# Optimization experiments

Measured on AMD Instinct MI355X. Metric: run time of the kernel, lower is better.

The kernel has to match this reference:

```python
import math
import jax, jax.numpy as jnp
import numpy as np

B, T, D, N_SLOTS, TOP_K = 4, 4096, 2048, 4096, 4


def setup_inputs() -> dict:
    key = jax.random.key(0)
    k1, k2, k3, k4, k5 = jax.random.split(key, 5)
    return {
        "x": jax.random.normal(k1, (B, T, D), dtype=jnp.float32),
        "slot_keys": jax.random.normal(k2, (N_SLOTS, D), dtype=jnp.float32) * 0.02,
        "slot_values": jax.random.normal(k3, (N_SLOTS, D), dtype=jnp.float32) * 0.02,
        "Wq": jax.random.normal(k4, (D, D), dtype=jnp.float32) * 0.02,
        "Wout": jax.random.normal(k5, (D, D), dtype=jnp.float32) * 0.02,
        "top_k": TOP_K,
    }


def reference(x, slot_keys, slot_values, Wq, Wout, top_k):
    d = x.shape[-1]
    scale = 1.0 / math.sqrt(d)
    q = jnp.einsum("btd,ed->bte", x, Wq)                 # proj_q (Linear, no bias)
    scores = jnp.einsum("btd,nd->btn", q, slot_keys) * scale  # [B,T,n_slots]
    topk_vals, topk_ids = jax.lax.top_k(scores, top_k)   # [B,T,k]
    attn = jax.nn.softmax(topk_vals, axis=-1)            # [B,T,k]
    gathered = slot_values[topk_ids]                     # [B,T,k,D] gather
    retrieved = jnp.einsum("btk,btkd->btd", attn, gathered)
    return jnp.einsum("btd,ed->bte", retrieved, Wout)    # proj_out
```

## Files before the change

kernel.cpp:

```cpp
#include <hip/hip_runtime.h>
#include <math.h>

#define D_DIM    2048
#define BT_DIM   16384
#define NSLOTS   4096
#define NTILES   32
#define SCALE    0.02209708691207961f
#define MARGIN   0.02f
#define CAND_MAX 16

typedef __attribute__((ext_vector_type(8))) short bf16x8;
typedef __attribute__((ext_vector_type(4))) float f32x4;
typedef __attribute__((ext_vector_type(8))) unsigned short u16x8;
typedef __attribute__((ext_vector_type(4))) unsigned short u16x4;

__device__ __forceinline__ unsigned short f2bf(float f) {
    unsigned int u = __float_as_uint(f);
    return (unsigned short)((u + 0x7fffu + ((u >> 16) & 1u)) >> 16);
}
__device__ __forceinline__ float bf2f(unsigned short s) {
    return __uint_as_float(((unsigned int)s) << 16);
}

__device__ __forceinline__ void async_cp16(const void* g, void* l) {
    __builtin_amdgcn_global_load_lds(
        (const __attribute__((address_space(1))) void*)g,
        (__attribute__((address_space(3))) void*)l, 16, 0, 0);
}

__device__ __forceinline__ bool cand_better(float v, int i, float v2, int i2) {
    return (v > v2) || (v == v2 && i < i2);
}

__device__ __forceinline__ void cand_insert(float v, int idx,
                                            float& v0, int& i0, float& v1, int& i1,
                                            float& v2, int& i2, float& v3, int& i3) {
    if (cand_better(v, idx, v3, i3)) {
        if (cand_better(v, idx, v0, i0)) {
            v3 = v2; i3 = i2; v2 = v1; i2 = i1; v1 = v0; i1 = i0; v0 = v; i0 = idx;
        } else if (cand_better(v, idx, v1, i1)) {
            v3 = v2; i3 = i2; v2 = v1; i2 = i1; v1 = v; i1 = idx;
        } else if (cand_better(v, idx, v2, i2)) {
            v3 = v2; i3 = i2; v2 = v; i2 = idx;
        } else {
            v3 = v; i3 = idx;
        }
    }
}

__device__ __forceinline__ void split3v(float v, unsigned short& h,
                                        unsigned short& m, unsigned short& l) {
    h = f2bf(v);
    const float r1 = v - bf2f(h);
    m = f2bf(r1);
    l = f2bf(r1 - bf2f(m));
}

__global__ __launch_bounds__(256)
void split3_lin(const float* __restrict__ in, unsigned short* __restrict__ oh,
                unsigned short* __restrict__ om, unsigned short* __restrict__ ol) {
    const size_t i = ((size_t)blockIdx.x * 256 + threadIdx.x) * 4;
    const float4 v = *(const float4*)(in + i);
    u16x4 h, m, l;
    unsigned short th, tm, tl;
    split3v(v.x, th, tm, tl); h[0] = th; m[0] = tm; l[0] = tl;
    split3v(v.y, th, tm, tl); h[1] = th; m[1] = tm; l[1] = tl;
    split3v(v.z, th, tm, tl); h[2] = th; m[2] = tm; l[2] = tl;
    split3v(v.w, th, tm, tl); h[3] = th; m[3] = tm; l[3] = tl;
    *(u16x4*)(oh + i) = h;
    *(u16x4*)(om + i) = m;
    *(u16x4*)(ol + i) = l;
}

__global__ __launch_bounds__(256)
void split3_wqT(const float* __restrict__ W, unsigned short* __restrict__ th,
                unsigned short* __restrict__ tm, unsigned short* __restrict__ tl) {
    __shared__ float tile[32][33];
    const int tx  = threadIdx.x & 31;
    const int ty4 = (threadIdx.x >> 5) * 4;
    const int e0  = blockIdx.y * 32;
    const int d0  = blockIdx.x * 32;
#pragma unroll
    for (int r = 0; r < 4; ++r)
        tile[ty4 + r][tx] = W[(size_t)(e0 + ty4 + r) * D_DIM + (d0 + tx)];
    __syncthreads();
#pragma unroll
    for (int r = 0; r < 4; ++r) {
        const float v = tile[tx][ty4 + r];
        unsigned short h, m, l;
        split3v(v, h, m, l);
        const size_t o = (size_t)(d0 + ty4 + r) * D_DIM + (e0 + tx);
        th[o] = h; tm[o] = m; tl[o] = l;
    }
}

__global__ __launch_bounds__(256)
void cvt_f32_bf16(const float* __restrict__ in, unsigned short* __restrict__ out) {
    const size_t i = ((size_t)blockIdx.x * 256 + threadIdx.x) * 8;
    float4 a = *(const float4*)(in + i);
    float4 b = *(const float4*)(in + i + 4);
    u16x8 o;
    o[0] = f2bf(a.x); o[1] = f2bf(a.y); o[2] = f2bf(a.z); o[3] = f2bf(a.w);
    o[4] = f2bf(b.x); o[5] = f2bf(b.y); o[6] = f2bf(b.z); o[7] = f2bf(b.w);
    *(u16x8*)(out + i) = o;
}

__global__ __launch_bounds__(256)
void gemm_kw_mfma6(const unsigned short* __restrict__ Ah,
                   const unsigned short* __restrict__ Am,
                   const unsigned short* __restrict__ Al,
                   const unsigned short* __restrict__ Bh,
                   const unsigned short* __restrict__ Bm,
                   const unsigned short* __restrict__ Bl,
                   float* __restrict__ KW, unsigned short* __restrict__ kwb,
                   int M, int N, int K) {
    __shared__ __align__(16) unsigned short AldsH[128 * 32];
    __shared__ __align__(16) unsigned short AldsM[128 * 32];
    __shared__ __align__(16) unsigned short AldsL[128 * 32];
    __shared__ __align__(16) unsigned short BldsH[128 * 32];
    __shared__ __align__(16) unsigned short BldsM[128 * 32];
    __shared__ __align__(16) unsigned short BldsL[128 * 32];

    const int tid  = threadIdx.x;
    const int lane = tid & 63;
    const int w    = tid >> 6;
    const int wr   = w >> 1, wc = w & 1;
    const int bmr  = blockIdx.y * 128;
    const int bnc  = blockIdx.x * 128;

    const int srow = lane >> 2;
    const int skch = (lane & 3) ^ ((lane >> 3) & 3);
    const int c0 = w, c1 = w + 4;
    size_t oA0 = (size_t)(bmr + c0 * 16 + srow) * K + skch * 8;
    size_t oA1 = (size_t)(bmr + c1 * 16 + srow) * K + skch * 8;
    size_t oB0 = (size_t)(bnc + c0 * 16 + srow) * K + skch * 8;
    size_t oB1 = (size_t)(bnc + c1 * 16 + srow) * K + skch * 8;
    char* lAh0 = (char*)AldsH + c0 * 1024;  char* lAh1 = (char*)AldsH + c1 * 1024;
    char* lAm0 = (char*)AldsM + c0 * 1024;  char* lAm1 = (char*)AldsM + c1 * 1024;
    char* lAl0 = (char*)AldsL + c0 * 1024;  char* lAl1 = (char*)AldsL + c1 * 1024;
    char* lBh0 = (char*)BldsH + c0 * 1024;  char* lBh1 = (char*)BldsH + c1 * 1024;
    char* lBm0 = (char*)BldsM + c0 * 1024;  char* lBm1 = (char*)BldsM + c1 * 1024;
    char* lBl0 = (char*)BldsL + c0 * 1024;  char* lBl1 = (char*)BldsL + c1 * 1024;

    const int kbyte = (((lane >> 4) ^ ((lane >> 1) & 3)) << 4);
    const int rA = wr * 64 + (lane & 15);
    const int rB = wc * 64 + (lane & 15);

    f32x4 acc[4][4] = {};

    for (int kt = 0; kt < K; kt += 32) {
        async_cp16(Ah + oA0, lAh0);  async_cp16(Ah + oA1, lAh1);
        async_cp16(Am + oA0, lAm0);  async_cp16(Am + oA1, lAm1);
        async_cp16(Al + oA0, lAl0);  async_cp16(Al + oA1, lAl1);
        async_cp16(Bh + oB0, lBh0);  async_cp16(Bh + oB1, lBh1);
        async_cp16(Bm + oB0, lBm0);  async_cp16(Bm + oB1, lBm1);
        async_cp16(Bl + oB0, lBl0);  async_cp16(Bl + oB1, lBl1);
        oA0 += 32; oA1 += 32; oB0 += 32; oB1 += 32;
        __syncthreads();

        bf16x8 afh[4], afm[4], afl[4], bfh[4], bfm[4], bfl[4];
#pragma unroll
        for (int i = 0; i < 4; ++i) {
            const int ar = (rA + i * 16) * 64 + kbyte;
            afh[i] = *(const bf16x8*)((const char*)AldsH + ar);
            afm[i] = *(const bf16x8*)((const char*)AldsM + ar);
            afl[i] = *(const bf16x8*)((const char*)AldsL + ar);
            const int br = (rB + i * 16) * 64 + kbyte;
            bfh[i] = *(const bf16x8*)((const char*)BldsH + br);
            bfm[i] = *(const bf16x8*)((const char*)BldsM + br);
            bfl[i] = *(const bf16x8*)((const char*)BldsL + br);
        }
#pragma unroll
        for (int i = 0; i < 4; ++i)
#pragma unroll
            for (int j = 0; j < 4; ++j) {
                f32x4 c = acc[i][j];
                c = __builtin_amdgcn_mfma_f32_16x16x32_bf16(afh[i], bfh[j], c, 0, 0, 0);
                c = __builtin_amdgcn_mfma_f32_16x16x32_bf16(afh[i], bfm[j], c, 0, 0, 0);
                c = __builtin_amdgcn_mfma_f32_16x16x32_bf16(afm[i], bfh[j], c, 0, 0, 0);
                c = __builtin_amdgcn_mfma_f32_16x16x32_bf16(afm[i], bfm[j], c, 0, 0, 0);
                c = __builtin_amdgcn_mfma_f32_16x16x32_bf16(afh[i], bfl[j], c, 0, 0, 0);
                c = __builtin_amdgcn_mfma_f32_16x16x32_bf16(afl[i], bfh[j], c, 0, 0, 0);
                acc[i][j] = c;
            }
        __syncthreads();
    }

    const int orow = (lane >> 4) * 4;
    const int ocol = lane & 15;
#pragma unroll
    for (int i = 0; i < 4; ++i)
#pragma unroll
        for (int j = 0; j < 4; ++j) {
            const size_t base =
                (size_t)(bmr + wr * 64 + i * 16 + orow) * N + (bnc + wc * 64 + j * 16 + ocol);
#pragma unroll
            for (int r = 0; r < 4; ++r) {
                const float v = acc[i][j][r];
                KW[base + (size_t)r * N]  = v;
                kwb[base + (size_t)r * N] = f2bf(v);
            }
        }
}

template <bool BF16_OUT>
__global__ __launch_bounds__(256)
void gemm_bf16_abt(const unsigned short* __restrict__ A,
                   const unsigned short* __restrict__ B,
                   void* __restrict__ Cv, int M, int N, int K) {
    __shared__ __align__(16) unsigned short Alds[128 * 32];
    __shared__ __align__(16) unsigned short Blds[128 * 32];

    const int tid  = threadIdx.x;
    const int lane = tid & 63;
    const int w    = tid >> 6;
    const int wr   = w >> 1, wc = w & 1;
    const int bm   = blockIdx.y * 128;
    const int bn   = blockIdx.x * 128;

    const int srow = lane >> 2;
    const int skch = (lane & 3) ^ ((lane >> 3) & 3);
    const int c0 = w, c1 = w + 4;
    const unsigned short* gA0 = A + (size_t)(bm + c0 * 16 + srow) * K + skch * 8;
    const unsigned short* gA1 = A + (size_t)(bm + c1 * 16 + srow) * K + skch * 8;
    const unsigned short* gB0 = B + (size_t)(bn + c0 * 16 + srow) * K + skch * 8;
    const unsigned short* gB1 = B + (size_t)(bn + c1 * 16 + srow) * K + skch * 8;
    char* lA0 = (char*)Alds + c0 * 1024;
    char* lA1 = (char*)Alds + c1 * 1024;
    char* lB0 = (char*)Blds + c0 * 1024;
    char* lB1 = (char*)Blds + c1 * 1024;

    const int kbyte = (((lane >> 4) ^ ((lane >> 1) & 3)) << 4);
    const int rA = wr * 64 + (lane & 15);
    const int rB = wc * 64 + (lane & 15);

    f32x4 acc[4][4] = {};

    for (int kt = 0; kt < K; kt += 32) {
        async_cp16(gA0, lA0);
        async_cp16(gA1, lA1);
        async_cp16(gB0, lB0);
        async_cp16(gB1, lB1);
        gA0 += 32; gA1 += 32; gB0 += 32; gB1 += 32;
        __syncthreads();

        bf16x8 a[4], b[4];
#pragma unroll
        for (int i = 0; i < 4; ++i) {
            a[i] = *(const bf16x8*)((const char*)Alds + (rA + i * 16) * 64 + kbyte);
            b[i] = *(const bf16x8*)((const char*)Blds + (rB + i * 16) * 64 + kbyte);
        }
#pragma unroll
        for (int i = 0; i < 4; ++i)
#pragma unroll
            for (int j = 0; j < 4; ++j)
                acc[i][j] = __builtin_amdgcn_mfma_f32_16x16x32_bf16(
                    a[i], b[j], acc[i][j], 0, 0, 0);
        __syncthreads();
    }

    const int orow = (lane >> 4) * 4;
    const int ocol = lane & 15;
#pragma unroll
    for (int i = 0; i < 4; ++i)
#pragma unroll
        for (int j = 0; j < 4; ++j) {
            const size_t base =
                (size_t)(bm + wr * 64 + i * 16 + orow) * N + (bn + wc * 64 + j * 16 + ocol);
#pragma unroll
            for (int r = 0; r < 4; ++r) {
                if constexpr (BF16_OUT)
                    ((unsigned short*)Cv)[base + (size_t)r * N] = f2bf(acc[i][j][r]);
                else
                    ((float*)Cv)[base + (size_t)r * N] = acc[i][j][r];
            }
        }
}

__global__ __launch_bounds__(256)
void aux_pass(const unsigned short* __restrict__ scoresb,
              float4* __restrict__ aux) {
    const int tid  = threadIdx.x;
    const int lane = tid & 63;
    const int w    = tid >> 6;
    const int t    = blockIdx.x * 4 + w;
    const unsigned short* srow = scoresb + (size_t)t * NSLOTS;

#pragma unroll
    for (int j = 0; j < 8; ++j) {
        const int c0 = j * 512 + lane * 8;
        const u16x8 s8 = *(const u16x8*)(srow + c0);
        unsigned int k[8];
#pragma unroll
        for (int e = 0; e < 8; ++e) {
            const unsigned int b   = (unsigned int)s8[e] & 0xffffu;
            const unsigned int ord = b ^ ((b & 0x8000u) ? 0xffffu : 0x8000u);
            k[e] = (ord << 12) | (4095u - (unsigned int)(c0 + e));
        }
        unsigned int win[4];
#pragma unroll
        for (int p = 0; p < 4; ++p) {
            unsigned int m01 = max(k[0], k[1]), m23 = max(k[2], k[3]);
            unsigned int m45 = max(k[4], k[5]), m67 = max(k[6], k[7]);
            unsigned int m = max(max(m01, m23), max(m45, m67));
#pragma unroll
            for (int off = 1; off < 16; off <<= 1)
                m = max(m, (unsigned int)__shfl_xor((int)m, off));
            win[p] = m;
#pragma unroll
            for (int e = 0; e < 8; ++e) k[e] = (k[e] == m) ? 0u : k[e];
        }
        if ((lane & 15) == 0) {
            float vv[4]; int id[4];
#pragma unroll
            for (int p = 0; p < 4; ++p) {
                const unsigned int ord = win[p] >> 12;
                const unsigned int b =
                    (ord & 0x8000u) ? (ord ^ 0x8000u) : (~ord & 0xffffu);
                vv[p] = bf2f((unsigned short)b);
                id[p] = 4095 - (int)(win[p] & 0xfffu);
            }
            const int tile = j * 4 + (lane >> 4);
            float4* dst = aux + ((size_t)t * NTILES + tile) * 2;
            float4 o1, o2;
            o1.x = vv[0]; o1.y = __int_as_float(id[0]);
            o1.z = vv[1]; o1.w = __int_as_float(id[1]);
            o2.x = vv[2]; o2.y = __int_as_float(id[2]);
            o2.z = vv[3]; o2.w = __int_as_float(id[3]);
            dst[0] = o1;
            dst[1] = o2;
        }
    }
}

__global__ __launch_bounds__(256)
void topk_refine(const float4* __restrict__ aux,
                 const unsigned short* __restrict__ scoresb,
                 const float* __restrict__ x,
                 const float* __restrict__ KW,
                 const unsigned short* __restrict__ svb,
                 unsigned short* __restrict__ retr) {
    const int tid  = threadIdx.x;
    const int lane = tid & 63;
    const int w    = tid >> 6;
    const int t    = blockIdx.x * 4 + w;

    const float* xrow = x + (size_t)t * D_DIM + lane * 4;
    float4 xv[8];
#pragma unroll
    for (int i = 0; i < 8; ++i) xv[i] = *(const float4*)(xrow + 256 * i);

    __shared__ int          cand[4][CAND_MAX];
    __shared__ int          ncand[4];
    __shared__ unsigned int flags[4];
    if (lane == 0) { ncand[w] = 0; flags[w] = 0; }
    __syncthreads();

    const float4 e2 = aux[(size_t)t * 64 + lane];
    float v0 = -INFINITY, v1 = -INFINITY, v2 = -INFINITY, v3 = -INFINITY;
    int   i0 = 0x7fffffff, i1 = 0x7fffffff, i2 = 0x7fffffff, i3 = 0x7fffffff;
    cand_insert(e2.x, __float_as_int(e2.y), v0, i0, v1, i1, v2, i2, v3, i3);
    cand_insert(e2.z, __float_as_int(e2.w), v0, i0, v1, i1, v2, i2, v3, i3);
#pragma unroll
    for (int off = 1; off < 64; off <<= 1) {
        float s0 = __shfl_xor(v0, off), s1 = __shfl_xor(v1, off);
        float s2 = __shfl_xor(v2, off), s3 = __shfl_xor(v3, off);
        int   j0 = __shfl_xor(i0, off), j1 = __shfl_xor(i1, off);
        int   j2 = __shfl_xor(i2, off), j3 = __shfl_xor(i3, off);
        cand_insert(s0, j0, v0, i0, v1, i1, v2, i2, v3, i3);
        cand_insert(s1, j1, v0, i0, v1, i1, v2, i2, v3, i3);
        cand_insert(s2, j2, v0, i0, v1, i1, v2, i2, v3, i3);
        cand_insert(s3, j3, v0, i0, v1, i1, v2, i2, v3, i3);
    }
    const float thresh = v3 - MARGIN;

    if ((lane & 1) && e2.z >= thresh)
        atomicOr(&flags[w], 1u << (lane >> 1));
    __syncthreads();
    const unsigned int fl = flags[w];

    const int mytile = lane >> 1;
    if (!((fl >> mytile) & 1u)) {
        if (e2.x >= thresh) {
            int p = atomicAdd(&ncand[w], 1);
            if (p < CAND_MAX) cand[w][p] = __float_as_int(e2.y);
        }
        if (e2.z >= thresh) {
            int p = atomicAdd(&ncand[w], 1);
            if (p < CAND_MAX) cand[w][p] = __float_as_int(e2.w);
        }
    }
    unsigned int fscan = fl;
    while (fscan) {
        const int tb = __ffs(fscan) - 1;
        fscan &= fscan - 1;
        const unsigned short* srow =
            scoresb + (size_t)t * NSLOTS + tb * 128 + lane * 2;
        const unsigned short s0 = srow[0], s1 = srow[1];
        if (bf2f(s0) >= thresh) {
            int p = atomicAdd(&ncand[w], 1);
            if (p < CAND_MAX) cand[w][p] = tb * 128 + lane * 2;
        }
        if (bf2f(s1) >= thresh) {
            int p = atomicAdd(&ncand[w], 1);
            if (p < CAND_MAX) cand[w][p] = tb * 128 + lane * 2 + 1;
        }
    }
    __syncthreads();
    const int nc = min(ncand[w], CAND_MAX);

    float r0 = -INFINITY, r1 = -INFINITY, r2 = -INFINITY, r3 = -INFINITY;
    int   q0 = 0x7fffffff, q1 = 0x7fffffff, q2 = 0x7fffffff, q3 = 0x7fffffff;
    for (int c = 0; c < nc; ++c) {
        const int slot = cand[w][c];
        const float* kr = KW + (size_t)slot * D_DIM + lane * 4;
        float p = 0.0f;
#pragma unroll
        for (int i = 0; i < 8; ++i) {
            const float4 k4 = *(const float4*)(kr + 256 * i);
            p = fmaf(xv[i].x, k4.x, p);
            p = fmaf(xv[i].y, k4.y, p);
            p = fmaf(xv[i].z, k4.z, p);
            p = fmaf(xv[i].w, k4.w, p);
        }
#pragma unroll
        for (int off = 1; off < 64; off <<= 1) p += __shfl_xor(p, off);
        cand_insert(p, slot, r0, q0, r1, q1, r2, q2, r3, q3);
    }

    const float e1s = expf(SCALE * (r1 - r0));
    const float e2s = expf(SCALE * (r2 - r0));
    const float e3s = expf(SCALE * (r3 - r0));
    const float inv = 1.0f / (1.0f + e1s + e2s + e3s);
    const float w0s = inv, w1s = e1s * inv, w2s = e2s * inv, w3s = e3s * inv;

    const unsigned short* p0 = svb + (size_t)q0 * D_DIM;
    const unsigned short* p1 = svb + (size_t)q1 * D_DIM;
    const unsigned short* p2 = svb + (size_t)q2 * D_DIM;
    const unsigned short* p3 = svb + (size_t)q3 * D_DIM;
    unsigned short* orow = retr + (size_t)t * D_DIM;
#pragma unroll
    for (int i = 0; i < 4; ++i) {
        const int d0 = lane * 8 + 512 * i;
        u16x8 a0 = *(const u16x8*)(p0 + d0);
        u16x8 a1 = *(const u16x8*)(p1 + d0);
        u16x8 a2 = *(const u16x8*)(p2 + d0);
        u16x8 a3 = *(const u16x8*)(p3 + d0);
        u16x8 o;
#pragma unroll
        for (int e = 0; e < 8; ++e) {
            float s = w0s * bf2f(a0[e]) + w1s * bf2f(a1[e]) +
                      w2s * bf2f(a2[e]) + w3s * bf2f(a3[e]);
            o[e] = f2bf(s);
        }
        *(u16x8*)(orow + d0) = o;
    }
}

extern "C" void kernel_launch(void* const* d_in, const int* in_sizes, int n_in,
                              void* d_out, int out_size, void* d_ws, size_t ws_size,
                              hipStream_t stream) {
    const float* x    = (const float*)d_in[0];
    const float* sk   = (const float*)d_in[1];
    const float* sv   = (const float*)d_in[2];
    const float* wq   = (const float*)d_in[3];
    const float* wout = (const float*)d_in[4];

    char* base = (char*)d_ws;
    unsigned short* scoresb = (unsigned short*)base;
    float*          KW      = (float*)(base + 134217728);
    unsigned short* kwb     = (unsigned short*)(base + 167772160);
    unsigned short* woutb   = (unsigned short*)(base + 184549376);
    unsigned short* xb      = (unsigned short*)(base + 192937984);
    unsigned short* svb     = (unsigned short*)(base + 260046848);
    float4*         aux     = (float4*)(base + 276824064);
    unsigned short* skh     = (unsigned short*)(base + 293601280);
    unsigned short* skm     = (unsigned short*)(base + 310378496);
    unsigned short* skl     = (unsigned short*)(base + 327155712);
    unsigned short* wqth    = (unsigned short*)(base + 343932928);
    unsigned short* wqtm    = (unsigned short*)(base + 352321536);
    unsigned short* wqtl    = (unsigned short*)(base + 360710144);

    const dim3 blk(256);

    split3_lin<<<dim3((NSLOTS * (size_t)D_DIM) / 1024), blk, 0, stream>>>(
        sk, skh, skm, skl);
    split3_wqT<<<dim3(D_DIM / 32, D_DIM / 32), blk, 0, stream>>>(
        wq, wqth, wqtm, wqtl);

    cvt_f32_bf16<<<dim3((BT_DIM * (size_t)D_DIM) / 2048), blk, 0, stream>>>(x, xb);
    cvt_f32_bf16<<<dim3((D_DIM * (size_t)D_DIM) / 2048), blk, 0, stream>>>(wout, woutb);
    cvt_f32_bf16<<<dim3((NSLOTS * (size_t)D_DIM) / 2048), blk, 0, stream>>>(sv, svb);

    gemm_kw_mfma6<<<dim3(D_DIM / 128, NSLOTS / 128), blk, 0, stream>>>(
        skh, skm, skl, wqth, wqtm, wqtl, KW, kwb, NSLOTS, D_DIM, D_DIM);

    gemm_bf16_abt<true><<<dim3(NSLOTS / 128, BT_DIM / 128), blk, 0, stream>>>(
        xb, kwb, scoresb, BT_DIM, NSLOTS, D_DIM);

    aux_pass<<<dim3(BT_DIM / 4), blk, 0, stream>>>(scoresb, aux);

    topk_refine<<<dim3(BT_DIM / 4), blk, 0, stream>>>(
        aux, scoresb, x, KW, svb, xb);

    gemm_bf16_abt<false><<<dim3(D_DIM / 128, BT_DIM / 128), blk, 0, stream>>>(
        xb, woutb, (float*)d_out, BT_DIM, D_DIM, D_DIM);
}
```

Measured before the change: 1.066 ms.

## Fuse per-tile top-k aux pass into refine kernel with register-resident row scan

Removes the separate aux_pass kernel and its aux buffer. Each wavefront now loads its whole bf16 score row into 64 registers per lane, finds the exact bf16 top-4 with wave-wide max reductions, then collects every slot within the margin as a candidate for fp32 rescoring. This drops one kernel launch and the write and re-read of the aux array, plus the tile-rescan path. In exchange it raises register pressure, which may lower occupancy, and it loops over all 64 elements per lane when gathering candidates.

```diff
diff --git a/kernel.cpp b/kernel.cpp
--- a/kernel.cpp
+++ b/kernel.cpp
@@ -4,7 +4,6 @@
 #define D_DIM    2048
 #define BT_DIM   16384
 #define NSLOTS   4096
-#define NTILES   32
 #define SCALE    0.02209708691207961f
 #define MARGIN   0.02f
 #define CAND_MAX 16
@@ -278,64 +277,7 @@
 }
 
 __global__ __launch_bounds__(256)
-void aux_pass(const unsigned short* __restrict__ scoresb,
-              float4* __restrict__ aux) {
-    const int tid  = threadIdx.x;
-    const int lane = tid & 63;
-    const int w    = tid >> 6;
-    const int t    = blockIdx.x * 4 + w;
-    const unsigned short* srow = scoresb + (size_t)t * NSLOTS;
-
-#pragma unroll
-    for (int j = 0; j < 8; ++j) {
-        const int c0 = j * 512 + lane * 8;
-        const u16x8 s8 = *(const u16x8*)(srow + c0);
-        unsigned int k[8];
-#pragma unroll
-        for (int e = 0; e < 8; ++e) {
-            const unsigned int b   = (unsigned int)s8[e] & 0xffffu;
-            const unsigned int ord = b ^ ((b & 0x8000u) ? 0xffffu : 0x8000u);
-            k[e] = (ord << 12) | (4095u - (unsigned int)(c0 + e));
-        }
-        unsigned int win[4];
-#pragma unroll
-        for (int p = 0; p < 4; ++p) {
-            unsigned int m01 = max(k[0], k[1]), m23 = max(k[2], k[3]);
-            unsigned int m45 = max(k[4], k[5]), m67 = max(k[6], k[7]);
-            unsigned int m = max(max(m01, m23), max(m45, m67));
-#pragma unroll
-            for (int off = 1; off < 16; off <<= 1)
-                m = max(m, (unsigned int)__shfl_xor((int)m, off));
-            win[p] = m;
-#pragma unroll
-            for (int e = 0; e < 8; ++e) k[e] = (k[e] == m) ? 0u : k[e];
-        }
-        if ((lane & 15) == 0) {
-            float vv[4]; int id[4];
-#pragma unroll
-            for (int p = 0; p < 4; ++p) {
-                const unsigned int ord = win[p] >> 12;
-                const unsigned int b =
-                    (ord & 0x8000u) ? (ord ^ 0x8000u) : (~ord & 0xffffu);
-                vv[p] = bf2f((unsigned short)b);
-                id[p] = 4095 - (int)(win[p] & 0xfffu);
-            }
-            const int tile = j * 4 + (lane >> 4);
-            float4* dst = aux + ((size_t)t * NTILES + tile) * 2;
-            float4 o1, o2;
-            o1.x = vv[0]; o1.y = __int_as_float(id[0]);
-            o1.z = vv[1]; o1.w = __int_as_float(id[1]);
-            o2.x = vv[2]; o2.y = __int_as_float(id[2]);
-            o2.z = vv[3]; o2.w = __int_as_float(id[3]);
-            dst[0] = o1;
-            dst[1] = o2;
-        }
-    }
-}
-
-__global__ __launch_bounds__(256)
-void topk_refine(const float4* __restrict__ aux,
-                 const unsigned short* __restrict__ scoresb,
+void topk_refine(const unsigned short* __restrict__ scoresb,
                  const float* __restrict__ x,
                  const float* __restrict__ KW,
                  const unsigned short* __restrict__ svb,
@@ -344,70 +286,76 @@
     const int lane = tid & 63;
     const int w    = tid >> 6;
     const int t    = blockIdx.x * 4 + w;
+    const unsigned short* srow = scoresb + (size_t)t * NSLOTS;
+
+    __shared__ int cand[4][CAND_MAX];
+    __shared__ int ncand[4];
+
+    unsigned int k[64];
+#pragma unroll
+    for (int j = 0; j < 8; ++j) {
+        const int c0 = j * 512 + lane * 8;
+        const u16x8 s8 = *(const u16x8*)(srow + c0);
+#pragma unroll
+        for (int e = 0; e < 8; ++e) {
+            const unsigned int b   = (unsigned int)s8[e] & 0xffffu;
+            const unsigned int ord = b ^ ((b & 0x8000u) ? 0xffffu : 0x8000u);
+            k[j * 8 + e] = (ord << 12) | (4095u - (unsigned int)(c0 + e));
+        }
+    }
+
+    unsigned int win[4];
+#pragma unroll
+    for (int p = 0; p < 4; ++p) {
+        unsigned int a16[16];
+#pragma unroll
+        for (int e = 0; e < 16; ++e)
+            a16[e] = max(max(k[e], k[e + 16]), max(k[e + 32], k[e + 48]));
+        unsigned int a4[4];
+#pragma unroll
+        for (int e = 0; e < 4; ++e)
+            a4[e] = max(max(a16[e], a16[e + 4]), max(a16[e + 8], a16[e + 12]));
+        unsigned int m = max(max(a4[0], a4[1]), max(a4[2], a4[3]));
+#pragma unroll
+        for (int off = 1; off < 64; off <<= 1)
+            m = max(m, (unsigned int)__shfl_xor((int)m, off));
+        win[p] = m;
+#pragma unroll
+        for (int e = 0; e < 64; ++e) k[e] = (k[e] == m) ? 0u : k[e];
+    }
+
+    const unsigned int ord3 = win[3] >> 12;
+    const unsigned int b3 =
+        (ord3 & 0x8000u) ? (ord3 ^ 0x8000u) : (~ord3 & 0xffffu);
+    const float thresh = bf2f((unsigned short)b3) - MARGIN;
+
+    if (lane == 0) {
+        ncand[w] = 4;
+        cand[w][0] = 4095 - (int)(win[0] & 0xfffu);
+        cand[w][1] = 4095 - (int)(win[1] & 0xfffu);
+        cand[w][2] = 4095 - (int)(win[2] & 0xfffu);
+        cand[w][3] = 4095 - (int)(win[3] & 0xfffu);
+    }
+    __syncthreads();
+
+#pragma unroll
+    for (int e = 0; e < 64; ++e) {
+        const unsigned int kk  = k[e];
+        const unsigned int ordv = kk >> 12;
+        const unsigned int bv =
+            (ordv & 0x8000u) ? (ordv ^ 0x8000u) : (~ordv & 0xffffu);
+        if (bf2f((unsigned short)bv) >= thresh) {
+            int p = atomicAdd(&ncand[w], 1);
+            if (p < CAND_MAX) cand[w][p] = 4095 - (int)(kk & 0xfffu);
+        }
+    }
+    __syncthreads();
+    const int nc = min(ncand[w], CAND_MAX);
 
     const float* xrow = x + (size_t)t * D_DIM + lane * 4;
     float4 xv[8];
 #pragma unroll
     for (int i = 0; i < 8; ++i) xv[i] = *(const float4*)(xrow + 256 * i);
-
-    __shared__ int          cand[4][CAND_MAX];
-    __shared__ int          ncand[4];
-    __shared__ unsigned int flags[4];
-    if (lane == 0) { ncand[w] = 0; flags[w] = 0; }
-    __syncthreads();
-
-    const float4 e2 = aux[(size_t)t * 64 + lane];
-    float v0 = -INFINITY, v1 = -INFINITY, v2 = -INFINITY, v3 = -INFINITY;
-    int   i0 = 0x7fffffff, i1 = 0x7fffffff, i2 = 0x7fffffff, i3 = 0x7fffffff;
-    cand_insert(e2.x, __float_as_int(e2.y), v0, i0, v1, i1, v2, i2, v3, i3);
-    cand_insert(e2.z, __float_as_int(e2.w), v0, i0, v1, i1, v2, i2, v3, i3);
-#pragma unroll
-    for (int off = 1; off < 64; off <<= 1) {
-        float s0 = __shfl_xor(v0, off), s1 = __shfl_xor(v1, off);
-        float s2 = __shfl_xor(v2, off), s3 = __shfl_xor(v3, off);
-        int   j0 = __shfl_xor(i0, off), j1 = __shfl_xor(i1, off);
-        int   j2 = __shfl_xor(i2, off), j3 = __shfl_xor(i3, off);
-        cand_insert(s0, j0, v0, i0, v1, i1, v2, i2, v3, i3);
-        cand_insert(s1, j1, v0, i0, v1, i1, v2, i2, v3, i3);
-        cand_insert(s2, j2, v0, i0, v1, i1, v2, i2, v3, i3);
-        cand_insert(s3, j3, v0, i0, v1, i1, v2, i2, v3, i3);
-    }
-    const float thresh = v3 - MARGIN;
-
-    if ((lane & 1) && e2.z >= thresh)
-        atomicOr(&flags[w], 1u << (lane >> 1));
-    __syncthreads();
-    const unsigned int fl = flags[w];
-
-    const int mytile = lane >> 1;
-    if (!((fl >> mytile) & 1u)) {
-        if (e2.x >= thresh) {
-            int p = atomicAdd(&ncand[w], 1);
-            if (p < CAND_MAX) cand[w][p] = __float_as_int(e2.y);
-        }
-        if (e2.z >= thresh) {
-            int p = atomicAdd(&ncand[w], 1);
-            if (p < CAND_MAX) cand[w][p] = __float_as_int(e2.w);
-        }
-    }
-    unsigned int fscan = fl;
-    while (fscan) {
-        const int tb = __ffs(fscan) - 1;
-        fscan &= fscan - 1;
-        const unsigned short* srow =
-            scoresb + (size_t)t * NSLOTS + tb * 128 + lane * 2;
-        const unsigned short s0 = srow[0], s1 = srow[1];
-        if (bf2f(s0) >= thresh) {
-            int p = atomicAdd(&ncand[w], 1);
-            if (p < CAND_MAX) cand[w][p] = tb * 128 + lane * 2;
-        }
-        if (bf2f(s1) >= thresh) {
-            int p = atomicAdd(&ncand[w], 1);
-            if (p < CAND_MAX) cand[w][p] = tb * 128 + lane * 2 + 1;
-        }
-    }
-    __syncthreads();
-    const int nc = min(ncand[w], CAND_MAX);
 
     float r0 = -INFINITY, r1 = -INFINITY, r2 = -INFINITY, r3 = -INFINITY;
     int   q0 = 0x7fffffff, q1 = 0x7fffffff, q2 = 0x7fffffff, q3 = 0x7fffffff;
@@ -473,7 +421,6 @@
     unsigned short* woutb   = (unsigned short*)(base + 184549376);
     unsigned short* xb      = (unsigned short*)(base + 192937984);
     unsigned short* svb     = (unsigned short*)(base + 260046848);
-    float4*         aux     = (float4*)(base + 276824064);
     unsigned short* skh     = (unsigned short*)(base + 293601280);
     unsigned short* skm     = (unsigned short*)(base + 310378496);
     unsigned short* skl     = (unsigned short*)(base + 327155712);
@@ -498,10 +445,8 @@
     gemm_bf16_abt<true><<<dim3(NSLOTS / 128, BT_DIM / 128), blk, 0, stream>>>(
         xb, kwb, scoresb, BT_DIM, NSLOTS, D_DIM);
 
-    aux_pass<<<dim3(BT_DIM / 4), blk, 0, stream>>>(scoresb, aux);
-
     topk_refine<<<dim3(BT_DIM / 4), blk, 0, stream>>>(
-        aux, scoresb, x, KW, svb, xb);
+        scoresb, x, KW, svb, xb);
 
     gemm_bf16_abt<false><<<dim3(D_DIM / 128, BT_DIM / 128), blk, 0, stream>>>(
         xb, woutb, (float*)d_out, BT_DIM, D_DIM, D_DIM);
```

Measured after the change: 989.1 us. -7.2%, faster.
